# Optimization experiments

Hardware: AMD Instinct MI355X
Metric: run time of the kernel (lower is better)

The kernel has to match this reference:

```python
import jax, jax.numpy as jnp
import numpy as np

TEMPERATURE = 10000.0


def _grid_sample_bilinear(img, ix, iy):
    """torch.nn.functional.grid_sample equivalent (bilinear, zero padding,
    align_corners=False), with pixel coords ix, iy already unnormalized.
    img: [B,C,H,W]; ix, iy: [B,K,H,W]. Returns [B,C,K,H,W]."""
    B, C, H, W = img.shape
    K = ix.shape[1]
    x0 = jnp.floor(ix)
    y0 = jnp.floor(iy)
    x1 = x0 + 1.0
    y1 = y0 + 1.0
    wx1 = ix - x0
    wx0 = 1.0 - wx1
    wy1 = iy - y0
    wy0 = 1.0 - wy1
    flat = img.reshape(B, C, H * W)

    def corner(xc, yc, w):
        valid = (xc >= 0) & (xc <= W - 1) & (yc >= 0) & (yc <= H - 1)
        xi = jnp.clip(xc, 0, W - 1).astype(jnp.int32)
        yi = jnp.clip(yc, 0, H - 1).astype(jnp.int32)
        idx = (yi * W + xi).reshape(B, 1, -1)  # [B,1,K*H*W]
        g = jnp.take_along_axis(flat, jnp.broadcast_to(idx, (B, C, idx.shape[-1])), axis=2)
        g = g.reshape(B, C, K, H, W)
        wv = (w * valid.astype(img.dtype)).reshape(B, 1, K, H, W)
        return g * wv

    return (corner(x0, y0, wx0 * wy0) + corner(x1, y0, wx1 * wy0)
            + corner(x0, y1, wx0 * wy1) + corner(x1, y1, wx1 * wy1))


def _forward(left_features, right_features, offset_x, offset_y):
    B, C, H, W = left_features.shape
    dt = left_features.dtype
    # left coordinate grids (buffers built in __init__)
    lx = jnp.arange(W, dtype=dt)[None, None, None, :]               # [1,1,1,W]
    # faithful to original: y coords clamped to max = W-1 (no-op when H<=W)
    ly = jnp.clip(jnp.arange(H, dtype=dt), 0, W - 1)[None, None, :, None]  # [1,1,H,1]

    rx = jnp.clip(lx - offset_x, 0.0, W - 1.0)                      # [B,K,H,W]
    ry = jnp.clip(ly - offset_y, 0.0, H - 1.0)                      # [B,K,H,W]
    # normalize to [-1,1] as in original
    gx = (rx - W / 2) / (W / 2)
    gy = (ry - H / 2) / (H / 2)
    # unnormalize per align_corners=False convention
    ix = ((gx + 1.0) * W - 1.0) * 0.5
    iy = ((gy + 1.0) * H - 1.0) * 0.5

    sampled = _grid_sample_bilinear(right_features, ix, iy)         # [B,C,K,H,W]
    strength = jnp.mean(-jnp.abs(left_features[:, :, None] - sampled), axis=1) * TEMPERATURE  # [B,K,H,W]
    w = jax.nn.softmax(strength, axis=1)
    ox = jnp.sum(offset_x * w, axis=1, keepdims=True)               # [B,1,H,W]
    oy = jnp.sum(offset_y * w, axis=1, keepdims=True)               # [B,1,H,W]
    return ox, oy


def setup_inputs() -> dict:
    key = jax.random.key(0)
    k1, k2, k3, k4 = jax.random.split(key, 4)
    B, C, H, W, K = 1, 32, 256, 512, 10
    left_features = jax.random.normal(k1, (B, C, H, W), jnp.float32)
    right_features = jax.random.normal(k2, (B, C, H, W), jnp.float32)
    # horizontal disparity candidates in [0, 64) px; small vertical jitter
    offset_x = jax.random.uniform(k3, (B, K, H, W), jnp.float32) * 64.0
    offset_y = jax.random.normal(k4, (B, K, H, W), jnp.float32) * 2.0
    return {"left_features": left_features, "right_features": right_features,
            "offset_x": offset_x, "offset_y": offset_y}


def reference(left_features, right_features, offset_x, offset_y):
    return _forward(left_features, right_features, offset_x, offset_y)
```

## Files before the change

### kernel.cpp

```cpp
#include <hip/hip_runtime.h>

constexpr int C = 32, H = 256, W = 512, K = 10;
constexpr int HW = H * W;
constexpr float TEMP = 10000.0f;

__global__ __launch_bounds__(256) void conv_right_hwc(
    const float* __restrict__ in, float* __restrict__ out)
{
    __shared__ float t[C][129];
    const int base = blockIdx.x * 128;
    const int tid = threadIdx.x;
    #pragma unroll
    for (int i = 0; i < 16; ++i) {
        int lin = i * 256 + tid;
        int c = lin >> 7, px = lin & 127;
        t[c][px] = in[c * HW + base + px];
    }
    __syncthreads();
    #pragma unroll
    for (int i = 0; i < 16; ++i) {
        int lin = i * 256 + tid;
        int px = lin >> 5, c = lin & 31;
        out[(base + px) * C + c] = t[c][px];
    }
}

struct Frag {
    float4 a0, a1, b0, b1, d0, d1, e0, e1;
    float w00, w01, w10, w11;
};

__device__ __forceinline__ Frag load_frag(const float4* __restrict__ rb, int q,
                                          float lx, float ly, float ox, float oy)
{
    Frag f;
    float rx = fminf(fmaxf(lx - ox, 0.0f), (float)(W - 1));
    float ry = fminf(fmaxf(ly - oy, 0.0f), (float)(H - 1));
    float gx = (rx - (float)(W / 2)) / (float)(W / 2);
    float gy = (ry - (float)(H / 2)) / (float)(H / 2);
    float ix = ((gx + 1.0f) * (float)W - 1.0f) * 0.5f;
    float iy = ((gy + 1.0f) * (float)H - 1.0f) * 0.5f;

    float x0f = floorf(ix), y0f = floorf(iy);
    float wx1 = ix - x0f, wy1 = iy - y0f;
    float wx0 = 1.0f - wx1, wy0 = 1.0f - wy1;
    int x0 = (int)x0f, y0 = (int)y0f;

    float ax = (x0 >= 0) ? wx0 : 0.0f;
    float ay = (y0 >= 0) ? wy0 : 0.0f;
    f.w00 = ax * ay;   f.w01 = wx1 * ay;
    f.w10 = ax * wy1;  f.w11 = wx1 * wy1;

    int xi0 = max(x0, 0), yi0 = max(y0, 0);
    int xi1 = x0 + 1,     yi1 = y0 + 1;
    int r0 = yi0 * W, r1 = yi1 * W;
    int b00 = (r0 + xi0) * 8 + q;
    int b01 = (r0 + xi1) * 8 + q;
    int b10 = (r1 + xi0) * 8 + q;
    int b11 = (r1 + xi1) * 8 + q;
    f.a0 = rb[b00]; f.a1 = rb[b00 + 4];
    f.b0 = rb[b01]; f.b1 = rb[b01 + 4];
    f.d0 = rb[b10]; f.d1 = rb[b10 + 4];
    f.e0 = rb[b11]; f.e1 = rb[b11 + 4];
    return f;
}

__device__ __forceinline__ float consume(const Frag& f, const float lf[8])
{
    float acc = 0.0f;
    acc += fabsf(lf[0] - (f.w00 * f.a0.x + f.w01 * f.b0.x + f.w10 * f.d0.x + f.w11 * f.e0.x));
    acc += fabsf(lf[1] - (f.w00 * f.a0.y + f.w01 * f.b0.y + f.w10 * f.d0.y + f.w11 * f.e0.y));
    acc += fabsf(lf[2] - (f.w00 * f.a0.z + f.w01 * f.b0.z + f.w10 * f.d0.z + f.w11 * f.e0.z));
    acc += fabsf(lf[3] - (f.w00 * f.a0.w + f.w01 * f.b0.w + f.w10 * f.d0.w + f.w11 * f.e0.w));
    acc += fabsf(lf[4] - (f.w00 * f.a1.x + f.w01 * f.b1.x + f.w10 * f.d1.x + f.w11 * f.e1.x));
    acc += fabsf(lf[5] - (f.w00 * f.a1.y + f.w01 * f.b1.y + f.w10 * f.d1.y + f.w11 * f.e1.y));
    acc += fabsf(lf[6] - (f.w00 * f.a1.z + f.w01 * f.b1.z + f.w10 * f.d1.z + f.w11 * f.e1.z));
    acc += fabsf(lf[7] - (f.w00 * f.a1.w + f.w01 * f.b1.w + f.w10 * f.d1.w + f.w11 * f.e1.w));
    return acc;
}

__global__ __launch_bounds__(256, 4) void disp_kernel_hwc(
    const float* __restrict__ lchw, const float* __restrict__ rhwc,
    const float* __restrict__ offx, const float* __restrict__ offy,
    float* __restrict__ out)
{
    const int tid = threadIdx.x;
    const int q = tid & 3;
    const int p = blockIdx.x * 64 + (tid >> 2);
    const int w = p & (W - 1);
    const int h = p >> 9;

    float lf[8];
    #pragma unroll
    for (int j = 0; j < 4; ++j) lf[j]     = lchw[(4 * q + j) * HW + p];
    #pragma unroll
    for (int j = 0; j < 4; ++j) lf[4 + j] = lchw[(16 + 4 * q + j) * HW + p];

    float okx[K], oky[K];
    #pragma unroll
    for (int k = 0; k < K; ++k) {
        okx[k] = offx[k * HW + p];
        oky[k] = offy[k * HW + p];
    }

    const float lx = (float)w;
    const float ly = (float)h;
    const float4* rb = (const float4*)rhwc;

    float s[K];
    Frag cur = load_frag(rb, q, lx, ly, okx[0], oky[0]);

    #pragma unroll
    for (int k = 0; k < K; ++k) {
        Frag nxt;
        if (k + 1 < K) nxt = load_frag(rb, q, lx, ly, okx[k + 1], oky[k + 1]);
        float acc = consume(cur, lf);
        acc += __shfl_xor(acc, 1);
        acc += __shfl_xor(acc, 2);
        s[k] = acc * (-TEMP / (float)C);
        if (k + 1 < K) cur = nxt;
    }

    float m = s[0];
    #pragma unroll
    for (int k = 1; k < K; ++k) m = fmaxf(m, s[k]);
    float den = 0.0f, sx = 0.0f, sy = 0.0f;
    #pragma unroll
    for (int k = 0; k < K; ++k) {
        float e = __expf(s[k] - m);
        den += e;
        sx += okx[k] * e;
        sy += oky[k] * e;
    }
    float inv = 1.0f / den;
    if (q == 0) {
        out[p]      = sx * inv;
        out[HW + p] = sy * inv;
    }
}

__global__ __launch_bounds__(256) void disp_kernel_chw(
    const float* __restrict__ left, const float* __restrict__ right,
    const float* __restrict__ offx, const float* __restrict__ offy,
    float* __restrict__ out)
{
    const int p = blockIdx.x * 256 + threadIdx.x;
    const int w = p & (W - 1);
    const int h = p >> 9;
    float lf[C];
    #pragma unroll
    for (int c = 0; c < C; ++c) lf[c] = left[c * HW + p];
    const float lx = (float)w, ly = (float)h;
    float s[K], okx[K], oky[K];
    #pragma unroll
    for (int k = 0; k < K; ++k) {
        const float ox = offx[k * HW + p], oy = offy[k * HW + p];
        okx[k] = ox; oky[k] = oy;
        float rx = fminf(fmaxf(lx - ox, 0.0f), (float)(W - 1));
        float ry = fminf(fmaxf(ly - oy, 0.0f), (float)(H - 1));
        float gx = (rx - 256.0f) / 256.0f, gy = (ry - 128.0f) / 128.0f;
        float ix = ((gx + 1.0f) * (float)W - 1.0f) * 0.5f;
        float iy = ((gy + 1.0f) * (float)H - 1.0f) * 0.5f;
        float x0f = floorf(ix), y0f = floorf(iy);
        float wx1 = ix - x0f, wy1 = iy - y0f;
        float wx0 = 1.0f - wx1, wy0 = 1.0f - wy1;
        int x0 = (int)x0f, y0 = (int)y0f, x1 = x0 + 1, y1 = y0 + 1;
        float vx0 = (x0 >= 0) ? 1.0f : 0.0f;
        float vy0 = (y0 >= 0) ? 1.0f : 0.0f;
        float w00 = wx0 * wy0 * vx0 * vy0, w01 = wx1 * wy0 * vy0;
        float w10 = wx0 * wy1 * vx0, w11 = wx1 * wy1;
        int xi0 = max(x0, 0), xi1 = x1;
        int yi0 = max(y0, 0), yi1 = y1;
        int i00 = yi0 * W + xi0, i01 = yi0 * W + xi1;
        int i10 = yi1 * W + xi0, i11 = yi1 * W + xi1;
        float acc = 0.0f;
        #pragma unroll
        for (int c = 0; c < C; ++c) {
            const float* rc = right + c * HW;
            acc += fabsf(lf[c] - (w00 * rc[i00] + w01 * rc[i01]
                                + w10 * rc[i10] + w11 * rc[i11]));
        }
        s[k] = acc * (-TEMP / (float)C);
    }
    float m = s[0];
    #pragma unroll
    for (int k = 1; k < K; ++k) m = fmaxf(m, s[k]);
    float den = 0.0f, sx = 0.0f, sy = 0.0f;
    #pragma unroll
    for (int k = 0; k < K; ++k) {
        float e = __expf(s[k] - m);
        den += e; sx += okx[k] * e; sy += oky[k] * e;
    }
    float inv = 1.0f / den;
    out[p] = sx * inv;
    out[HW + p] = sy * inv;
}

extern "C" void kernel_launch(void* const* d_in, const int* in_sizes, int n_in,
                              void* d_out, int out_size, void* d_ws, size_t ws_size,
                              hipStream_t stream) {
    const float* left  = (const float*)d_in[0];
    const float* right = (const float*)d_in[1];
    const float* offx  = (const float*)d_in[2];
    const float* offy  = (const float*)d_in[3];
    float* out = (float*)d_out;

    const size_t need = (size_t)HW * C * sizeof(float);
    if (ws_size >= need) {
        float* rhwc = (float*)d_ws;
        conv_right_hwc<<<HW / 128, 256, 0, stream>>>(right, rhwc);
        disp_kernel_hwc<<<HW / 64, 256, 0, stream>>>(left, rhwc, offx, offy, out);
    } else {
        disp_kernel_chw<<<HW / 256, 256, 0, stream>>>(left, right, offx, offy, out);
    }
}
```

Measured before the change: 122.8 us.

## Split disparity candidates across two thread groups per pixel

```diff
diff --git a/kernel.cpp b/kernel.cpp
--- a/kernel.cpp
+++ b/kernel.cpp
@@ -25,68 +25,15 @@
     }
 }
 
-struct Frag {
-    float4 a0, a1, b0, b1, d0, d1, e0, e1;
-    float w00, w01, w10, w11;
-};
-
-__device__ __forceinline__ Frag load_frag(const float4* __restrict__ rb, int q,
-                                          float lx, float ly, float ox, float oy)
-{
-    Frag f;
-    float rx = fminf(fmaxf(lx - ox, 0.0f), (float)(W - 1));
-    float ry = fminf(fmaxf(ly - oy, 0.0f), (float)(H - 1));
-    float gx = (rx - (float)(W / 2)) / (float)(W / 2);
-    float gy = (ry - (float)(H / 2)) / (float)(H / 2);
-    float ix = ((gx + 1.0f) * (float)W - 1.0f) * 0.5f;
-    float iy = ((gy + 1.0f) * (float)H - 1.0f) * 0.5f;
-
-    float x0f = floorf(ix), y0f = floorf(iy);
-    float wx1 = ix - x0f, wy1 = iy - y0f;
-    float wx0 = 1.0f - wx1, wy0 = 1.0f - wy1;
-    int x0 = (int)x0f, y0 = (int)y0f;
-
-    float ax = (x0 >= 0) ? wx0 : 0.0f;
-    float ay = (y0 >= 0) ? wy0 : 0.0f;
-    f.w00 = ax * ay;   f.w01 = wx1 * ay;
-    f.w10 = ax * wy1;  f.w11 = wx1 * wy1;
-
-    int xi0 = max(x0, 0), yi0 = max(y0, 0);
-    int xi1 = x0 + 1,     yi1 = y0 + 1;
-    int r0 = yi0 * W, r1 = yi1 * W;
-    int b00 = (r0 + xi0) * 8 + q;
-    int b01 = (r0 + xi1) * 8 + q;
-    int b10 = (r1 + xi0) * 8 + q;
-    int b11 = (r1 + xi1) * 8 + q;
-    f.a0 = rb[b00]; f.a1 = rb[b00 + 4];
-    f.b0 = rb[b01]; f.b1 = rb[b01 + 4];
-    f.d0 = rb[b10]; f.d1 = rb[b10 + 4];
-    f.e0 = rb[b11]; f.e1 = rb[b11 + 4];
-    return f;
-}
-
-__device__ __forceinline__ float consume(const Frag& f, const float lf[8])
-{
-    float acc = 0.0f;
-    acc += fabsf(lf[0] - (f.w00 * f.a0.x + f.w01 * f.b0.x + f.w10 * f.d0.x + f.w11 * f.e0.x));
-    acc += fabsf(lf[1] - (f.w00 * f.a0.y + f.w01 * f.b0.y + f.w10 * f.d0.y + f.w11 * f.e0.y));
-    acc += fabsf(lf[2] - (f.w00 * f.a0.z + f.w01 * f.b0.z + f.w10 * f.d0.z + f.w11 * f.e0.z));
-    acc += fabsf(lf[3] - (f.w00 * f.a0.w + f.w01 * f.b0.w + f.w10 * f.d0.w + f.w11 * f.e0.w));
-    acc += fabsf(lf[4] - (f.w00 * f.a1.x + f.w01 * f.b1.x + f.w10 * f.d1.x + f.w11 * f.e1.x));
-    acc += fabsf(lf[5] - (f.w00 * f.a1.y + f.w01 * f.b1.y + f.w10 * f.d1.y + f.w11 * f.e1.y));
-    acc += fabsf(lf[6] - (f.w00 * f.a1.z + f.w01 * f.b1.z + f.w10 * f.d1.z + f.w11 * f.e1.z));
-    acc += fabsf(lf[7] - (f.w00 * f.a1.w + f.w01 * f.b1.w + f.w10 * f.d1.w + f.w11 * f.e1.w));
-    return acc;
-}
-
-__global__ __launch_bounds__(256, 4) void disp_kernel_hwc(
+__global__ __launch_bounds__(256) void disp_kernel_hwc8(
     const float* __restrict__ lchw, const float* __restrict__ rhwc,
     const float* __restrict__ offx, const float* __restrict__ offy,
     float* __restrict__ out)
 {
     const int tid = threadIdx.x;
-    const int q = tid & 3;
-    const int p = blockIdx.x * 64 + (tid >> 2);
+    const int q  = tid & 3;
+    const int kk = (tid >> 2) & 1;
+    const int p  = blockIdx.x * 32 + (tid >> 3);
     const int w = p & (W - 1);
     const int h = p >> 9;
 
@@ -96,44 +43,82 @@
     #pragma unroll
     for (int j = 0; j < 4; ++j) lf[4 + j] = lchw[(16 + 4 * q + j) * HW + p];
 
-    float okx[K], oky[K];
-    #pragma unroll
-    for (int k = 0; k < K; ++k) {
-        okx[k] = offx[k * HW + p];
-        oky[k] = offy[k * HW + p];
-    }
-
     const float lx = (float)w;
     const float ly = (float)h;
     const float4* rb = (const float4*)rhwc;
 
-    float s[K];
-    Frag cur = load_frag(rb, q, lx, ly, okx[0], oky[0]);
+    float s[5];
 
     #pragma unroll
-    for (int k = 0; k < K; ++k) {
-        Frag nxt;
-        if (k + 1 < K) nxt = load_frag(rb, q, lx, ly, okx[k + 1], oky[k + 1]);
-        float acc = consume(cur, lf);
+    for (int j = 0; j < 5; ++j) {
+        const int k = 2 * j + kk;
+        const float ox = offx[k * HW + p];
+        const float oy = offy[k * HW + p];
+
+        float rx = fminf(fmaxf(lx - ox, 0.0f), (float)(W - 1));
+        float ry = fminf(fmaxf(ly - oy, 0.0f), (float)(H - 1));
+        float gx = (rx - (float)(W / 2)) / (float)(W / 2);
+        float gy = (ry - (float)(H / 2)) / (float)(H / 2);
+        float ix = ((gx + 1.0f) * (float)W - 1.0f) * 0.5f;
+        float iy = ((gy + 1.0f) * (float)H - 1.0f) * 0.5f;
+
+        float x0f = floorf(ix), y0f = floorf(iy);
+        float wx1 = ix - x0f, wy1 = iy - y0f;
+        float wx0 = 1.0f - wx1, wy0 = 1.0f - wy1;
+        int x0 = (int)x0f, y0 = (int)y0f;
+
+        float ax = (x0 >= 0) ? wx0 : 0.0f;
+        float ay = (y0 >= 0) ? wy0 : 0.0f;
+        float w00 = ax * ay,   w01 = wx1 * ay;
+        float w10 = ax * wy1,  w11 = wx1 * wy1;
+
+        int xi0 = max(x0, 0), yi0 = max(y0, 0);
+        int r0 = yi0 * W, r1 = (y0 + 1) * W;
+        int b00 = (r0 + xi0) * 8 + q;
+        int b01 = (r0 + x0 + 1) * 8 + q;
+        int b10 = (r1 + xi0) * 8 + q;
+        int b11 = (r1 + x0 + 1) * 8 + q;
+
+        float4 a0 = rb[b00], a1 = rb[b00 + 4];
+        float4 b0 = rb[b01], b1 = rb[b01 + 4];
+        float4 d0 = rb[b10], d1 = rb[b10 + 4];
+        float4 e0 = rb[b11], e1 = rb[b11 + 4];
+
+        float acc = 0.0f;
+        acc += fabsf(lf[0] - (w00 * a0.x + w01 * b0.x + w10 * d0.x + w11 * e0.x));
+        acc += fabsf(lf[1] - (w00 * a0.y + w01 * b0.y + w10 * d0.y + w11 * e0.y));
+        acc += fabsf(lf[2] - (w00 * a0.z + w01 * b0.z + w10 * d0.z + w11 * e0.z));
+        acc += fabsf(lf[3] - (w00 * a0.w + w01 * b0.w + w10 * d0.w + w11 * e0.w));
+        acc += fabsf(lf[4] - (w00 * a1.x + w01 * b1.x + w10 * d1.x + w11 * e1.x));
+        acc += fabsf(lf[5] - (w00 * a1.y + w01 * b1.y + w10 * d1.y + w11 * e1.y));
+        acc += fabsf(lf[6] - (w00 * a1.z + w01 * b1.z + w10 * d1.z + w11 * e1.z));
+        acc += fabsf(lf[7] - (w00 * a1.w + w01 * b1.w + w10 * d1.w + w11 * e1.w));
+
         acc += __shfl_xor(acc, 1);
         acc += __shfl_xor(acc, 2);
-        s[k] = acc * (-TEMP / (float)C);
-        if (k + 1 < K) cur = nxt;
+        s[j] = acc * (-TEMP / (float)C);
     }
 
     float m = s[0];
     #pragma unroll
-    for (int k = 1; k < K; ++k) m = fmaxf(m, s[k]);
+    for (int j = 1; j < 5; ++j) m = fmaxf(m, s[j]);
+    m = fmaxf(m, __shfl_xor(m, 4));
+
     float den = 0.0f, sx = 0.0f, sy = 0.0f;
     #pragma unroll
-    for (int k = 0; k < K; ++k) {
-        float e = __expf(s[k] - m);
+    for (int j = 0; j < 5; ++j) {
+        const int k = 2 * j + kk;
+        float e = __expf(s[j] - m);
         den += e;
-        sx += okx[k] * e;
-        sy += oky[k] * e;
+        sx += offx[k * HW + p] * e;
+        sy += offy[k * HW + p] * e;
     }
+    den += __shfl_xor(den, 4);
+    sx  += __shfl_xor(sx, 4);
+    sy  += __shfl_xor(sy, 4);
+
     float inv = 1.0f / den;
-    if (q == 0) {
+    if ((tid & 7) == 0) {
         out[p]      = sx * inv;
         out[HW + p] = sy * inv;
     }
@@ -164,15 +149,13 @@
         float x0f = floorf(ix), y0f = floorf(iy);
         float wx1 = ix - x0f, wy1 = iy - y0f;
         float wx0 = 1.0f - wx1, wy0 = 1.0f - wy1;
-        int x0 = (int)x0f, y0 = (int)y0f, x1 = x0 + 1, y1 = y0 + 1;
-        float vx0 = (x0 >= 0) ? 1.0f : 0.0f;
-        float vy0 = (y0 >= 0) ? 1.0f : 0.0f;
-        float w00 = wx0 * wy0 * vx0 * vy0, w01 = wx1 * wy0 * vy0;
-        float w10 = wx0 * wy1 * vx0, w11 = wx1 * wy1;
-        int xi0 = max(x0, 0), xi1 = x1;
-        int yi0 = max(y0, 0), yi1 = y1;
-        int i00 = yi0 * W + xi0, i01 = yi0 * W + xi1;
-        int i10 = yi1 * W + xi0, i11 = yi1 * W + xi1;
+        int x0 = (int)x0f, y0 = (int)y0f;
+        float ax = (x0 >= 0) ? wx0 : 0.0f;
+        float ay = (y0 >= 0) ? wy0 : 0.0f;
+        float w00 = ax * ay, w01 = wx1 * ay, w10 = ax * wy1, w11 = wx1 * wy1;
+        int xi0 = max(x0, 0), yi0 = max(y0, 0);
+        int i00 = yi0 * W + xi0, i01 = yi0 * W + x0 + 1;
+        int i10 = (y0 + 1) * W + xi0, i11 = (y0 + 1) * W + x0 + 1;
         float acc = 0.0f;
         #pragma unroll
         for (int c = 0; c < C; ++c) {
@@ -209,7 +192,7 @@
     if (ws_size >= need) {
         float* rhwc = (float*)d_ws;
         conv_right_hwc<<<HW / 128, 256, 0, stream>>>(right, rhwc);
-        disp_kernel_hwc<<<HW / 64, 256, 0, stream>>>(left, rhwc, offx, offy, out);
+        disp_kernel_hwc8<<<HW / 32, 256, 0, stream>>>(left, rhwc, offx, offy, out);
     } else {
         disp_kernel_chw<<<HW / 256, 256, 0, stream>>>(left, right, offx, offy, out);
     }
```

Result: slower. 126.7 us (+3.2%).
